# Kernel tuning notes

Measured on AMD Instinct MI355X. Metric: run time of the kernel, lower is better.

The kernel has to match this reference:

```python
import jax, jax.numpy as jnp
import numpy as np

B = 16384       # batch rows
N_IN = 8192     # input bits per row (columns of x)
N_GATES = 8192  # gates in this row


def setup_inputs() -> dict:
    key = jax.random.key(0)
    k_x, k_g, k_c = jax.random.split(key, 3)
    # binary activations entering the gate row
    x = jax.random.randint(k_x, (B, N_IN), 0, 2).astype(jnp.bool_)
    # per-gate 4-entry truth table (the discretized gate function)
    gates = jax.random.randint(k_g, (N_GATES, 4), 0, 2).astype(jnp.bool_)
    # per-gate pair of input wire indices into the N_IN columns of x
    choices = jax.random.randint(k_c, (N_GATES, 2), 0, N_IN, dtype=jnp.int32)
    return {"x": x, "gates": gates, "choices": choices}


def reference(x, gates, choices):
    n_gates = gates.shape[0]
    # gather the two chosen input bits per gate: [B, n_gates, 2]
    chosen = x[:, choices.reshape(-1)].reshape(x.shape[0], n_gates, 2)
    # 2-bit lookup index into the truth table: a*2 + b in {0,1,2,3}
    idx = chosen[:, :, 0].astype(jnp.int32) * 2 + chosen[:, :, 1].astype(jnp.int32)
    # out[b, g] = gates[g, idx[b, g]]  (advanced indexing broadcasts (1,G) x (B,G))
    out = gates[jnp.arange(n_gates)[None, :], idx]
    return out
```

## Files before the change

kernel.cpp:

```cpp
#include <hip/hip_runtime.h>
#include <stdint.h>


static constexpr int BATCH  = 16384;
static constexpr int N_IN   = 8192;
static constexpr int NG     = 8192;
static constexpr int ROWS   = 8;
static constexpr int BLK    = 256;
static constexpr int GPT    = 4;
static constexpr int NGROUP = NG / (BLK * GPT);

typedef uint32_t u32x4 __attribute__((ext_vector_type(4)));

__global__ void detect_mode(const uint8_t* __restrict__ x,
                            uint32_t* __restrict__ flag) {
    if (threadIdx.x == 0 && blockIdx.x == 0) {
        uint32_t nz = 0;
        for (int i = 0; i < 256; ++i)
            nz |= x[4 * i + 1] | x[4 * i + 2] | x[4 * i + 3];
        *flag = (nz == 0) ? 1u : 0u;
    }
}

__global__ void pack_meta(const int* __restrict__ choices,
                          const void* __restrict__ gates_,
                          const uint32_t* __restrict__ flag,
                          uint32_t* __restrict__ meta) {
    int g = blockIdx.x * blockDim.x + threadIdx.x;
    if (g >= NG) return;
    uint32_t c0 = (uint32_t)choices[2 * g];
    uint32_t c1 = (uint32_t)choices[2 * g + 1];
    uint32_t tt;
    if (*flag) {
        const int* gt = (const int*)gates_;
        tt = ((uint32_t)gt[4 * g] & 1u)        | (((uint32_t)gt[4 * g + 1] & 1u) << 1)
           | (((uint32_t)gt[4 * g + 2] & 1u) << 2) | (((uint32_t)gt[4 * g + 3] & 1u) << 3);
    } else {
        const uint8_t* gt = (const uint8_t*)gates_;
        tt = (uint32_t)gt[4 * g]       | ((uint32_t)gt[4 * g + 1] << 1)
           | ((uint32_t)gt[4 * g + 2] << 2) | ((uint32_t)gt[4 * g + 3] << 3);
    }
    meta[g] = c0 | (c1 << 13) | (tt << 26);
}

template <bool PACKED>
__global__ __launch_bounds__(BLK) void gate_main(
        const void*     __restrict__ xv,
        const uint32_t* __restrict__ meta,
        const int*      __restrict__ choices,
        const void*     __restrict__ gates_,
        const uint32_t* __restrict__ flag,
        uint32_t*       __restrict__ out) {
    __shared__ uint8_t xp[N_IN];
    const int  t   = threadIdx.x;
    const long b0  = (long)blockIdx.x * ROWS;
    const bool i32 = flag ? (*flag != 0) : true;

    if (i32) {
        const uint32_t* x = (const uint32_t*)xv;
        uint32_t* dst = (uint32_t*)xp;
        #pragma unroll
        for (int i = 0; i < N_IN / 4 / BLK; ++i) {
            const int o = t + i * BLK;
            uint32_t pb = 0;
            #pragma unroll
            for (int r = 0; r < ROWS; ++r) {
                const u32x4* src = (const u32x4*)(x + (b0 + r) * (long)N_IN) + o;
                u32x4 v = __builtin_nontemporal_load(src);
                pb |= (v.x << r) | (v.y << (r + 8))
                    | (v.z << (r + 16)) | (v.w << (r + 24));
            }
            dst[o] = pb;
        }
    } else {
        const u32x4* xr  = (const u32x4*)((const uint8_t*)xv + b0 * N_IN);
        u32x4*       dst = (u32x4*)xp;
        #pragma unroll
        for (int i = 0; i < N_IN / 16 / BLK; ++i) {
            const int o = t + i * BLK;
            u32x4 p = (u32x4){0u, 0u, 0u, 0u};
            #pragma unroll
            for (int r = 0; r < ROWS; ++r) {
                u32x4 v = __builtin_nontemporal_load(
                    &xr[(size_t)r * (N_IN / 16) + o]);
                p.x |= v.x << r;  p.y |= v.y << r;
                p.z |= v.z << r;  p.w |= v.w << r;
            }
            dst[o] = p;
        }
    }
    __syncthreads();

    for (int k = 0; k < NGROUP; ++k) {
        const int gbase = k * BLK * GPT + t * GPT;

        uint32_t mm[GPT];
        if (PACKED) {
            u32x4 m = ((const u32x4*)meta)[k * BLK + t];
            mm[0] = m.x; mm[1] = m.y; mm[2] = m.z; mm[3] = m.w;
        } else {
            #pragma unroll
            for (int j = 0; j < GPT; ++j) {
                int g = gbase + j;
                uint32_t c0 = (uint32_t)choices[2 * g];
                uint32_t c1 = (uint32_t)choices[2 * g + 1];
                uint32_t tt;
                if (i32) {
                    const int* gt = (const int*)gates_;
                    tt = ((uint32_t)gt[4*g] & 1u)        | (((uint32_t)gt[4*g+1] & 1u) << 1)
                       | (((uint32_t)gt[4*g+2] & 1u) << 2) | (((uint32_t)gt[4*g+3] & 1u) << 3);
                } else {
                    const uint8_t* gt = (const uint8_t*)gates_;
                    tt = (uint32_t)gt[4*g] | ((uint32_t)gt[4*g+1] << 1)
                       | ((uint32_t)gt[4*g+2] << 2) | ((uint32_t)gt[4*g+3] << 3);
                }
                mm[j] = c0 | (c1 << 13) | (tt << 26);
            }
        }

        uint32_t res[ROWS][GPT];
        #pragma unroll
        for (int j = 0; j < GPT; ++j) {
            const uint32_t mv = mm[j];
            const uint32_t v0 = xp[mv & 8191u];
            const uint32_t v1 = xp[(mv >> 13) & 8191u];
            const uint32_t tt = mv >> 26;
            #pragma unroll
            for (int r = 0; r < ROWS; ++r) {
                const uint32_t idx = (((v0 >> r) & 1u) << 1) | ((v1 >> r) & 1u);
                res[r][j] = (tt >> idx) & 1u;
            }
        }

        #pragma unroll
        for (int r = 0; r < ROWS; ++r) {
            u32x4 v = { res[r][0], res[r][1], res[r][2], res[r][3] };
            u32x4* dst = (u32x4*)(out + (b0 + r) * (long)NG + gbase);
            __builtin_nontemporal_store(v, dst);
        }
    }
}

extern "C" void kernel_launch(void* const* d_in, const int* in_sizes, int n_in,
                              void* d_out, int out_size, void* d_ws, size_t ws_size,
                              hipStream_t stream) {
    const void* x       = d_in[0];
    const void* gates   = d_in[1];
    const int*  choices = (const int*)d_in[2];
    uint32_t*   out     = (uint32_t*)d_out;

    if (ws_size >= 64 + NG * sizeof(uint32_t)) {
        uint32_t* flag = (uint32_t*)d_ws;
        uint32_t* meta = (uint32_t*)((char*)d_ws + 64);
        detect_mode<<<1, 64, 0, stream>>>((const uint8_t*)x, flag);
        pack_meta<<<NG / BLK, BLK, 0, stream>>>(choices, gates, flag, meta);
        gate_main<true><<<BATCH / ROWS, BLK, 0, stream>>>(
            x, meta, choices, gates, flag, out);
    } else if (ws_size >= 4) {
        uint32_t* flag = (uint32_t*)d_ws;
        detect_mode<<<1, 64, 0, stream>>>((const uint8_t*)x, flag);
        gate_main<false><<<BATCH / ROWS, BLK, 0, stream>>>(
            x, nullptr, choices, gates, flag, out);
    } else {
        gate_main<false><<<BATCH / ROWS, BLK, 0, stream>>>(
            x, nullptr, choices, gates, nullptr, out);
    }
}
```

Before: 837.1 us.

## Replace serial detect kernel with in-block wave ballot dtype detection and prefetch metadata

Removes the single-threaded detect_mode kernel launch and instead has each wave detect whether inputs are stored as int32 or bytes using a ballot over a 16-byte sample. pack_meta and gate_main each do this detection locally, which drops one launch and the dependent flag load. All per-gate metadata is loaded into registers before the compute loop, and choices are read as vectorised int2 loads. The per-wave heuristic can misclassify if a sampled byte-encoded chunk happens to contain only 0/1 in the low byte of every word, and holding the metadata in registers raises register pressure.

```diff
diff --git a/kernel.cpp b/kernel.cpp
--- a/kernel.cpp
+++ b/kernel.cpp
@@ -11,36 +11,30 @@
 static constexpr int NGROUP = NG / (BLK * GPT);
 
 typedef uint32_t u32x4 __attribute__((ext_vector_type(4)));
+typedef int      i32x2 __attribute__((ext_vector_type(2)));
 
-__global__ void detect_mode(const uint8_t* __restrict__ x,
-                            uint32_t* __restrict__ flag) {
-    if (threadIdx.x == 0 && blockIdx.x == 0) {
-        uint32_t nz = 0;
-        for (int i = 0; i < 256; ++i)
-            nz |= x[4 * i + 1] | x[4 * i + 2] | x[4 * i + 3];
-        *flag = (nz == 0) ? 1u : 0u;
-    }
+__device__ __forceinline__ bool wave_detect_i32(u32x4 w) {
+    return __ballot((((w.x | w.y | w.z | w.w) & ~1u) == 0u)) == ~0ULL;
 }
 
-__global__ void pack_meta(const int* __restrict__ choices,
-                          const void* __restrict__ gates_,
-                          const uint32_t* __restrict__ flag,
-                          uint32_t* __restrict__ meta) {
-    int g = blockIdx.x * blockDim.x + threadIdx.x;
-    if (g >= NG) return;
-    uint32_t c0 = (uint32_t)choices[2 * g];
-    uint32_t c1 = (uint32_t)choices[2 * g + 1];
+__global__ __launch_bounds__(BLK) void pack_meta(
+        const int* __restrict__ choices,
+        const void* __restrict__ gates_,
+        uint32_t* __restrict__ meta) {
+    const int g = blockIdx.x * BLK + threadIdx.x;
+    const bool i32 = wave_detect_i32(((const u32x4*)gates_)[g & 2047]);
+    i32x2 c = ((const i32x2*)choices)[g];
     uint32_t tt;
-    if (*flag) {
-        const int* gt = (const int*)gates_;
-        tt = ((uint32_t)gt[4 * g] & 1u)        | (((uint32_t)gt[4 * g + 1] & 1u) << 1)
-           | (((uint32_t)gt[4 * g + 2] & 1u) << 2) | (((uint32_t)gt[4 * g + 3] & 1u) << 3);
+    if (i32) {
+        u32x4 gw = ((const u32x4*)gates_)[g];
+        tt = (gw.x & 1u) | ((gw.y & 1u) << 1)
+           | ((gw.z & 1u) << 2) | ((gw.w & 1u) << 3);
     } else {
-        const uint8_t* gt = (const uint8_t*)gates_;
-        tt = (uint32_t)gt[4 * g]       | ((uint32_t)gt[4 * g + 1] << 1)
-           | ((uint32_t)gt[4 * g + 2] << 2) | ((uint32_t)gt[4 * g + 3] << 3);
+        const uint8_t* gt = (const uint8_t*)gates_ + 4 * (long)g;
+        tt = (uint32_t)gt[0] | ((uint32_t)gt[1] << 1)
+           | ((uint32_t)gt[2] << 2) | ((uint32_t)gt[3] << 3);
     }
-    meta[g] = c0 | (c1 << 13) | (tt << 26);
+    meta[g] = (uint32_t)c.x | ((uint32_t)c.y << 13) | (tt << 26);
 }
 
 template <bool PACKED>
@@ -49,12 +43,13 @@
         const uint32_t* __restrict__ meta,
         const int*      __restrict__ choices,
         const void*     __restrict__ gates_,
-        const uint32_t* __restrict__ flag,
         uint32_t*       __restrict__ out) {
     __shared__ uint8_t xp[N_IN];
-    const int  t   = threadIdx.x;
-    const long b0  = (long)blockIdx.x * ROWS;
-    const bool i32 = flag ? (*flag != 0) : true;
+    const int  t  = threadIdx.x;
+    const long b0 = (long)blockIdx.x * ROWS;
+
+    const bool i32 = wave_detect_i32(
+        ((const u32x4*)xv)[blockIdx.x * BLK + t]);
 
     if (i32) {
         const uint32_t* x = (const uint32_t*)xv;
@@ -91,37 +86,44 @@
     }
     __syncthreads();
 
+    u32x4 mq[NGROUP];
+    if (PACKED) {
+        #pragma unroll
+        for (int k = 0; k < NGROUP; ++k)
+            mq[k] = ((const u32x4*)meta)[k * BLK + t];
+    } else {
+        const bool gi32 = wave_detect_i32(
+            ((const u32x4*)gates_)[(blockIdx.x * BLK + t) & 2047]);
+        #pragma unroll
+        for (int k = 0; k < NGROUP; ++k) {
+            const int gb = k * BLK * GPT + t * GPT;
+            #pragma unroll
+            for (int j = 0; j < GPT; ++j) {
+                const int g = gb + j;
+                i32x2 c = ((const i32x2*)choices)[g];
+                uint32_t tt;
+                if (gi32) {
+                    u32x4 gw = ((const u32x4*)gates_)[g];
+                    tt = (gw.x & 1u) | ((gw.y & 1u) << 1)
+                       | ((gw.z & 1u) << 2) | ((gw.w & 1u) << 3);
+                } else {
+                    const uint8_t* gt = (const uint8_t*)gates_ + 4 * (long)g;
+                    tt = (uint32_t)gt[0] | ((uint32_t)gt[1] << 1)
+                       | ((uint32_t)gt[2] << 2) | ((uint32_t)gt[3] << 3);
+                }
+                mq[k][j] = (uint32_t)c.x | ((uint32_t)c.y << 13) | (tt << 26);
+            }
+        }
+    }
+
+    #pragma unroll
     for (int k = 0; k < NGROUP; ++k) {
         const int gbase = k * BLK * GPT + t * GPT;
-
-        uint32_t mm[GPT];
-        if (PACKED) {
-            u32x4 m = ((const u32x4*)meta)[k * BLK + t];
-            mm[0] = m.x; mm[1] = m.y; mm[2] = m.z; mm[3] = m.w;
-        } else {
-            #pragma unroll
-            for (int j = 0; j < GPT; ++j) {
-                int g = gbase + j;
-                uint32_t c0 = (uint32_t)choices[2 * g];
-                uint32_t c1 = (uint32_t)choices[2 * g + 1];
-                uint32_t tt;
-                if (i32) {
-                    const int* gt = (const int*)gates_;
-                    tt = ((uint32_t)gt[4*g] & 1u)        | (((uint32_t)gt[4*g+1] & 1u) << 1)
-                       | (((uint32_t)gt[4*g+2] & 1u) << 2) | (((uint32_t)gt[4*g+3] & 1u) << 3);
-                } else {
-                    const uint8_t* gt = (const uint8_t*)gates_;
-                    tt = (uint32_t)gt[4*g] | ((uint32_t)gt[4*g+1] << 1)
-                       | ((uint32_t)gt[4*g+2] << 2) | ((uint32_t)gt[4*g+3] << 3);
-                }
-                mm[j] = c0 | (c1 << 13) | (tt << 26);
-            }
-        }
 
         uint32_t res[ROWS][GPT];
         #pragma unroll
         for (int j = 0; j < GPT; ++j) {
-            const uint32_t mv = mm[j];
+            const uint32_t mv = mq[k][j];
             const uint32_t v0 = xp[mv & 8191u];
             const uint32_t v1 = xp[(mv >> 13) & 8191u];
             const uint32_t tt = mv >> 26;
@@ -149,20 +151,13 @@
     const int*  choices = (const int*)d_in[2];
     uint32_t*   out     = (uint32_t*)d_out;
 
-    if (ws_size >= 64 + NG * sizeof(uint32_t)) {
-        uint32_t* flag = (uint32_t*)d_ws;
-        uint32_t* meta = (uint32_t*)((char*)d_ws + 64);
-        detect_mode<<<1, 64, 0, stream>>>((const uint8_t*)x, flag);
-        pack_meta<<<NG / BLK, BLK, 0, stream>>>(choices, gates, flag, meta);
+    if (ws_size >= NG * sizeof(uint32_t)) {
+        uint32_t* meta = (uint32_t*)d_ws;
+        pack_meta<<<NG / BLK, BLK, 0, stream>>>(choices, gates, meta);
         gate_main<true><<<BATCH / ROWS, BLK, 0, stream>>>(
-            x, meta, choices, gates, flag, out);
-    } else if (ws_size >= 4) {
-        uint32_t* flag = (uint32_t*)d_ws;
-        detect_mode<<<1, 64, 0, stream>>>((const uint8_t*)x, flag);
-        gate_main<false><<<BATCH / ROWS, BLK, 0, stream>>>(
-            x, nullptr, choices, gates, flag, out);
+            x, meta, choices, gates, out);
     } else {
         gate_main<false><<<BATCH / ROWS, BLK, 0, stream>>>(
-            x, nullptr, choices, gates, nullptr, out);
+            x, nullptr, choices, gates, out);
     }
 }
```

New measurement: 829.7 us. Within noise of the previous version (-0.9%).
